# Performance work log

Hardware: AMD Instinct MI355X
Metric: run time of the kernel (lower is better)

The kernel has to match this reference:

```python
import jax, jax.numpy as jnp
import numpy as np


def setup_inputs() -> dict:
    key = jax.random.key(0)
    k1, k2 = jax.random.split(key)
    x = jax.random.normal(k1, (8, 128, 128, 128), dtype=jnp.float32)        # [N, C, H, W]
    codebook = jax.random.normal(k2, (256, 128), dtype=jnp.float32)         # [K, C] class_emb_vecs
    return {"x": x, "codebook": codebook}


def reference(x, codebook):
    # Brute-force 1-NN with p=2 (Euclidean), matching sklearn NearestNeighbors(brute, p=2).
    # argmin ||q - c||_2 == argmin (||q||^2 - 2 q.c + ||c||^2), so use the GEMM form.
    N, C, H, W = x.shape
    q = jnp.transpose(x, (0, 2, 3, 1)).reshape(-1, C)       # [N*H*W, C], matches x.reshape(-1, C) channel-last? 
    # NOTE: torch x.reshape(-1, C) on [N,C,H,W] flattens with C as the fastest-varying of the
    # leading dims only when memory layout is NCHW -> rows are (n, c_blocks)... Torch's
    # reshape(-1, C) actually slices contiguous groups of C elements along W. To be faithful
    # to x.reshape(-1, C) on a contiguous NCHW tensor:
    q = x.reshape(-1, C)                                     # [N*C*H*W/C, C] — same elements, same order as torch
    q_sq = jnp.sum(q * q, axis=1, keepdims=True)             # [M, 1]
    c_sq = jnp.sum(codebook * codebook, axis=1)              # [K]
    # squared distances: [M, K]
    d2 = q_sq - 2.0 * (q @ codebook.T) + c_sq[None, :]
    idx = jnp.argmin(d2, axis=1).astype(jnp.int32)           # [M]
    return idx.reshape(N, H, W)
```

## Files before the change

kernel.cpp:

```cpp
#include <hip/hip_runtime.h>
#include <hip/hip_bf16.h>


typedef __bf16 bf16x8 __attribute__((ext_vector_type(8)));
typedef float  floatx4 __attribute__((ext_vector_type(4)));

#define MFMA16 __builtin_amdgcn_mfma_f32_16x16x32_bf16

#define CNT_OFF 0
#define CSQ_OFF 1024
#define CBB_OFF 4096
#define WL_OFF  (4096 + 131072)
#define WL_CAP  32768
#define T_FLAG  0.004f

typedef __attribute__((address_space(1))) const unsigned int gu32;
typedef __attribute__((address_space(3))) unsigned int lu32;

__device__ __forceinline__ unsigned fmap(float f) {
    unsigned u = __float_as_uint(f);
    return (u & 0x80000000u) ? ~u : (u | 0x80000000u);
}

__global__ void knn_prep(const float* __restrict__ cb, __bf16* __restrict__ cbB,
                         float* __restrict__ csq, int* __restrict__ cnt) {
    const int tid = threadIdx.x;
    const int id = blockIdx.x * 256 + tid;
    if (id == 0) *cnt = 0;
    const int ln = id & 63;
    const int part = (id >> 6) & 1;
    const int step = id >> 7;
    const int t4 = step & 15;
    const int kb = step >> 4;
    const int n = t4 * 16 + (ln & 15);
    const int k0 = kb * 32 + (ln >> 4) * 8;
    const float* src = cb + (size_t)n * 128 + k0;
    union { __bf16 h[8]; uint4 u; } p;
#pragma unroll
    for (int j = 0; j < 8; ++j) {
        float f = src[j];
        __bf16 hh = (__bf16)f;
        p.h[j] = (part == 0) ? hh : (__bf16)(f - (float)hh);
    }
    *(uint4*)(cbB + (size_t)id * 8) = p.u;

    if (blockIdx.x == 0) {
        const float4* row = (const float4*)(cb + (size_t)tid * 128);
        float a0 = 0.f, a1 = 0.f, a2 = 0.f, a3 = 0.f;
#pragma unroll 8
        for (int j = 0; j < 32; ++j) {
            float4 v = row[j];
            a0 = fmaf(v.x, v.x, a0);
            a1 = fmaf(v.y, v.y, a1);
            a2 = fmaf(v.z, v.z, a2);
            a3 = fmaf(v.w, v.w, a3);
        }
        csq[tid] = (a0 + a1) + (a2 + a3);
    }
}

__global__ __launch_bounds__(512, 2) void knn_mfma(const float* __restrict__ x,
                                                   const __bf16* __restrict__ cbB,
                                                   const float* __restrict__ csq_g,
                                                   int* __restrict__ out,
                                                   int* __restrict__ cnt,
                                                   int* __restrict__ wl) {
    __shared__ __bf16 sB[65536];

    const int tid = threadIdx.x;
    const int wave = tid >> 6;
    const int lane = tid & 63;
    const int rl = lane & 15;
    const int kg = lane >> 4;

    {
        const char* gsrc = (const char*)cbB + wave * 16384 + lane * 16;
        char* ldst = (char*)sB + wave * 16384;
#pragma unroll
        for (int i = 0; i < 16; ++i)
            __builtin_amdgcn_global_load_lds((gu32*)(gsrc + i * 1024),
                                             (lu32*)(ldst + i * 1024), 16, 0, 0);
    }

    float cs[16];
#pragma unroll
    for (int t = 0; t < 16; ++t) cs[t] = csq_g[t * 16 + rl];

#pragma unroll 1
    for (int bt = 0; bt < 4; ++bt) {
        const size_t q0 = (size_t)blockIdx.x * 512 + bt * 128 + wave * 16;

        const float* xq = x + q0 * 128;
        bf16x8 ah[4], al[4];
#pragma unroll
        for (int kb = 0; kb < 4; ++kb) {
            const float* s = xq + (size_t)rl * 128 + kb * 32 + kg * 8;
            float4 f0 = *(const float4*)(s);
            float4 f1 = *(const float4*)(s + 4);
            float f[8] = {f0.x, f0.y, f0.z, f0.w, f1.x, f1.y, f1.z, f1.w};
            union { __bf16 h[8]; bf16x8 v; } ph, pl;
#pragma unroll
            for (int j = 0; j < 8; ++j) {
                __bf16 hh = (__bf16)f[j];
                ph.h[j] = hh;
                pl.h[j] = (__bf16)(f[j] - (float)hh);
            }
            ah[kb] = ph.v;
            al[kb] = pl.v;
        }

        floatx4 acc[16];
#pragma unroll
        for (int t = 0; t < 16; ++t) acc[t] = (floatx4){0.f, 0.f, 0.f, 0.f};

        if (bt == 0) __syncthreads();

#pragma unroll
        for (int kb = 0; kb < 4; ++kb) {
            const __bf16* sbase = sB + kb * 16384 + lane * 8;
#pragma unroll
            for (int t = 0; t < 16; ++t) {
                bf16x8 bh = *(const bf16x8*)(sbase + t * 1024);
                bf16x8 bl = *(const bf16x8*)(sbase + t * 1024 + 512);
                acc[t] = MFMA16(ah[kb], bh, acc[t], 0, 0, 0);
                acc[t] = MFMA16(al[kb], bh, acc[t], 0, 0, 0);
                acc[t] = MFMA16(ah[kb], bl, acc[t], 0, 0, 0);
            }
        }

#pragma unroll
        for (int r = 0; r < 4; ++r) {
            float bf = __builtin_inff(), sf = __builtin_inff();
            int bi = 0;
#pragma unroll
            for (int t = 0; t < 16; ++t) {
                const float sc = fmaf(-2.0f, acc[t][r], cs[t]);
                const bool lt = sc < bf;
                sf = lt ? bf : fminf(sf, sc);
                bf = lt ? sc : bf;
                bi = lt ? (t * 16 + rl) : bi;
            }
#pragma unroll
            for (int d = 1; d < 16; d <<= 1) {
                const float obf = __shfl_xor(bf, d);
                const int   obi = __shfl_xor(bi, d);
                const float osf = __shfl_xor(sf, d);
                const bool lt = obf < bf;
                const float loser = lt ? bf : obf;
                sf = fminf(fminf(sf, osf), loser);
                bf = lt ? obf : bf;
                bi = lt ? obi : bi;
            }
            if (rl == 0) {
                const size_t qg = q0 + kg * 4 + r;
                out[qg] = bi;
                if (sf - bf < T_FLAG) {
                    int idx = atomicAdd(cnt, 1);
                    if (idx < WL_CAP) wl[idx] = (int)qg;
                }
            }
        }
    }
}

__global__ __launch_bounds__(256) void knn_refine(const float* __restrict__ x,
                                                  const float* __restrict__ cb,
                                                  const float* __restrict__ csq_g,
                                                  const int* __restrict__ wl,
                                                  const int* __restrict__ cnt,
                                                  int* __restrict__ out) {
    __shared__ unsigned long long sP[4];
    const int tid = threadIdx.x;
    const int lane = tid & 63;
    const int wave = tid >> 6;

    int n = *cnt;
    if (n > WL_CAP) n = WL_CAP;
    const float mycsq = csq_g[tid];
    const float4* cr = (const float4*)(cb + (size_t)tid * 128);

    for (int i = blockIdx.x; i < n; i += gridDim.x) {
        const int q = wl[i];
        const float4* qr = (const float4*)(x + (size_t)q * 128);
        float a0 = 0.f, a1 = 0.f, a2 = 0.f, a3 = 0.f;
#pragma unroll 8
        for (int c4 = 0; c4 < 32; ++c4) {
            float4 qv = qr[c4];
            float4 cv = cr[c4];
            a0 = fmaf(qv.x, cv.x, a0);
            a1 = fmaf(qv.y, cv.y, a1);
            a2 = fmaf(qv.z, cv.z, a2);
            a3 = fmaf(qv.w, cv.w, a3);
        }
        float dot = (a0 + a1) + (a2 + a3);
        float score = fmaf(-2.0f, dot, mycsq);
        unsigned long long key =
            ((unsigned long long)fmap(score) << 32) | (unsigned)tid;
#pragma unroll
        for (int d = 1; d < 64; d <<= 1) {
            unsigned long long o = __shfl_xor(key, d);
            key = o < key ? o : key;
        }
        if (lane == 0) sP[wave] = key;
        __syncthreads();
        if (tid == 0) {
            unsigned long long b = sP[0];
            unsigned long long o;
            o = sP[1]; b = o < b ? o : b;
            o = sP[2]; b = o < b ? o : b;
            o = sP[3]; b = o < b ? o : b;
            out[q] = (int)(unsigned)(b & 0xFFFFFFFFull);
        }
        __syncthreads();
    }
}

extern "C" void kernel_launch(void* const* d_in, const int* in_sizes, int n_in,
                              void* d_out, int out_size, void* d_ws, size_t ws_size,
                              hipStream_t stream) {
    const float* x = (const float*)d_in[0];
    const float* cb = (const float*)d_in[1];
    int* out = (int*)d_out;

    char* ws = (char*)d_ws;
    int* cnt = (int*)(ws + CNT_OFF);
    float* csq = (float*)(ws + CSQ_OFF);
    __bf16* cbB = (__bf16*)(ws + CBB_OFF);
    int* wl = (int*)(ws + WL_OFF);

    const int M = in_sizes[0] / 128;

    knn_prep<<<32, 256, 0, stream>>>(cb, cbB, csq, cnt);
    knn_mfma<<<M / 512, 512, 0, stream>>>(x, cbB, csq, out, cnt, wl);
    knn_refine<<<240, 256, 0, stream>>>(x, cb, csq, wl, cnt, out);
}
```

Baseline: 121.9 us.

## Use 12 waves per block and fold codebook norms into MFMA accumulator init

Raises the block size of the main MFMA kernel from 8 to 12 waves. Each block still covers 512 queries, now as 32 tiles of 16 rows spread over 3 rounds, with the fourth-round waves masked off. The codebook LDS fill is redistributed across the 12 waves. Accumulators are seeded with -0.5*||c||^2 so the argmin becomes an argmax of the raw accumulator, which removes an FMA per score. The aim is more resident waves to hide latency, at the cost of fewer registers per thread and idle waves in the last round.

```diff
diff --git a/kernel.cpp b/kernel.cpp
--- a/kernel.cpp
+++ b/kernel.cpp
@@ -59,7 +59,7 @@
     }
 }
 
-__global__ __launch_bounds__(512, 2) void knn_mfma(const float* __restrict__ x,
+__global__ __launch_bounds__(768, 3) void knn_mfma(const float* __restrict__ x,
                                                    const __bf16* __restrict__ cbB,
                                                    const float* __restrict__ csq_g,
                                                    int* __restrict__ out,
@@ -73,13 +73,14 @@
     const int rl = lane & 15;
     const int kg = lane >> 4;
 
-    {
-        const char* gsrc = (const char*)cbB + wave * 16384 + lane * 16;
-        char* ldst = (char*)sB + wave * 16384;
-#pragma unroll
-        for (int i = 0; i < 16; ++i)
-            __builtin_amdgcn_global_load_lds((gu32*)(gsrc + i * 1024),
-                                             (lu32*)(ldst + i * 1024), 16, 0, 0);
+#pragma unroll
+    for (int i = 0; i < 11; ++i) {
+        const int c = wave + 12 * i;
+        if (c < 128) {
+            const char* g = (const char*)cbB + c * 1024 + lane * 16;
+            char* l = (char*)sB + c * 1024;
+            __builtin_amdgcn_global_load_lds((gu32*)g, (lu32*)l, 16, 0, 0);
+        }
     }
 
     float cs[16];
@@ -87,76 +88,85 @@
     for (int t = 0; t < 16; ++t) cs[t] = csq_g[t * 16 + rl];
 
 #pragma unroll 1
-    for (int bt = 0; bt < 4; ++bt) {
-        const size_t q0 = (size_t)blockIdx.x * 512 + bt * 128 + wave * 16;
-
-        const float* xq = x + q0 * 128;
+    for (int bt = 0; bt < 3; ++bt) {
+        const int c = bt * 12 + wave;
+        const bool valid = (c < 32);
+        const size_t q0 = (size_t)blockIdx.x * 512 + (size_t)c * 16;
+
         bf16x8 ah[4], al[4];
-#pragma unroll
-        for (int kb = 0; kb < 4; ++kb) {
-            const float* s = xq + (size_t)rl * 128 + kb * 32 + kg * 8;
-            float4 f0 = *(const float4*)(s);
-            float4 f1 = *(const float4*)(s + 4);
-            float f[8] = {f0.x, f0.y, f0.z, f0.w, f1.x, f1.y, f1.z, f1.w};
-            union { __bf16 h[8]; bf16x8 v; } ph, pl;
-#pragma unroll
-            for (int j = 0; j < 8; ++j) {
-                __bf16 hh = (__bf16)f[j];
-                ph.h[j] = hh;
-                pl.h[j] = (__bf16)(f[j] - (float)hh);
-            }
-            ah[kb] = ph.v;
-            al[kb] = pl.v;
-        }
-
         floatx4 acc[16];
-#pragma unroll
-        for (int t = 0; t < 16; ++t) acc[t] = (floatx4){0.f, 0.f, 0.f, 0.f};
+
+        if (valid) {
+            const float* xq = x + q0 * 128;
+#pragma unroll
+            for (int kb = 0; kb < 4; ++kb) {
+                const float* s = xq + (size_t)rl * 128 + kb * 32 + kg * 8;
+                float4 f0 = *(const float4*)(s);
+                float4 f1 = *(const float4*)(s + 4);
+                float f[8] = {f0.x, f0.y, f0.z, f0.w, f1.x, f1.y, f1.z, f1.w};
+                union { __bf16 h[8]; bf16x8 v; } ph, pl;
+#pragma unroll
+                for (int j = 0; j < 8; ++j) {
+                    __bf16 hh = (__bf16)f[j];
+                    ph.h[j] = hh;
+                    pl.h[j] = (__bf16)(f[j] - (float)hh);
+                }
+                ah[kb] = ph.v;
+                al[kb] = pl.v;
+            }
+#pragma unroll
+            for (int t = 0; t < 16; ++t) {
+                const float iv = -0.5f * cs[t];
+                acc[t] = (floatx4){iv, iv, iv, iv};
+            }
+        }
 
         if (bt == 0) __syncthreads();
 
-#pragma unroll
-        for (int kb = 0; kb < 4; ++kb) {
-            const __bf16* sbase = sB + kb * 16384 + lane * 8;
-#pragma unroll
-            for (int t = 0; t < 16; ++t) {
-                bf16x8 bh = *(const bf16x8*)(sbase + t * 1024);
-                bf16x8 bl = *(const bf16x8*)(sbase + t * 1024 + 512);
-                acc[t] = MFMA16(ah[kb], bh, acc[t], 0, 0, 0);
-                acc[t] = MFMA16(al[kb], bh, acc[t], 0, 0, 0);
-                acc[t] = MFMA16(ah[kb], bl, acc[t], 0, 0, 0);
-            }
-        }
-
-#pragma unroll
-        for (int r = 0; r < 4; ++r) {
-            float bf = __builtin_inff(), sf = __builtin_inff();
-            int bi = 0;
-#pragma unroll
-            for (int t = 0; t < 16; ++t) {
-                const float sc = fmaf(-2.0f, acc[t][r], cs[t]);
-                const bool lt = sc < bf;
-                sf = lt ? bf : fminf(sf, sc);
-                bf = lt ? sc : bf;
-                bi = lt ? (t * 16 + rl) : bi;
-            }
-#pragma unroll
-            for (int d = 1; d < 16; d <<= 1) {
-                const float obf = __shfl_xor(bf, d);
-                const int   obi = __shfl_xor(bi, d);
-                const float osf = __shfl_xor(sf, d);
-                const bool lt = obf < bf;
-                const float loser = lt ? bf : obf;
-                sf = fminf(fminf(sf, osf), loser);
-                bf = lt ? obf : bf;
-                bi = lt ? obi : bi;
-            }
-            if (rl == 0) {
-                const size_t qg = q0 + kg * 4 + r;
-                out[qg] = bi;
-                if (sf - bf < T_FLAG) {
-                    int idx = atomicAdd(cnt, 1);
-                    if (idx < WL_CAP) wl[idx] = (int)qg;
+        if (valid) {
+#pragma unroll
+            for (int kb = 0; kb < 4; ++kb) {
+                const __bf16* sbase = sB + kb * 16384 + lane * 8;
+#pragma unroll
+                for (int t = 0; t < 16; ++t) {
+                    bf16x8 bh = *(const bf16x8*)(sbase + t * 1024);
+                    bf16x8 bl = *(const bf16x8*)(sbase + t * 1024 + 512);
+                    acc[t] = MFMA16(ah[kb], bh, acc[t], 0, 0, 0);
+                    acc[t] = MFMA16(al[kb], bh, acc[t], 0, 0, 0);
+                    acc[t] = MFMA16(ah[kb], bl, acc[t], 0, 0, 0);
+                }
+            }
+
+#pragma unroll
+            for (int r = 0; r < 4; ++r) {
+                float bf = -__builtin_inff(), sf = -__builtin_inff();
+                int bi = 0;
+#pragma unroll
+                for (int t = 0; t < 16; ++t) {
+                    const float sc = acc[t][r];
+                    const bool gt = sc > bf;
+                    sf = gt ? bf : fmaxf(sf, sc);
+                    bf = gt ? sc : bf;
+                    bi = gt ? (t * 16 + rl) : bi;
+                }
+#pragma unroll
+                for (int d = 1; d < 16; d <<= 1) {
+                    const float obf = __shfl_xor(bf, d);
+                    const int   obi = __shfl_xor(bi, d);
+                    const float osf = __shfl_xor(sf, d);
+                    const bool gt = obf > bf;
+                    const float loser = gt ? bf : obf;
+                    sf = fmaxf(fmaxf(sf, osf), loser);
+                    bf = gt ? obf : bf;
+                    bi = gt ? obi : bi;
+                }
+                if (rl == 0) {
+                    const size_t qg = q0 + kg * 4 + r;
+                    out[qg] = bi;
+                    if (2.0f * (bf - sf) < T_FLAG) {
+                        int idx = atomicAdd(cnt, 1);
+                        if (idx < WL_CAP) wl[idx] = (int)qg;
+                    }
                 }
             }
         }
@@ -231,6 +241,6 @@
     const int M = in_sizes[0] / 128;
 
     knn_prep<<<32, 256, 0, stream>>>(cb, cbB, csq, cnt);
-    knn_mfma<<<M / 512, 512, 0, stream>>>(x, cbB, csq, out, cnt, wl);
+    knn_mfma<<<M / 512, 768, 0, stream>>>(x, cbB, csq, out, cnt, wl);
     knn_refine<<<240, 256, 0, stream>>>(x, cb, csq, wl, cnt, out);
 }
```

New measurement: 152.5 us. 25.1% more time.

## Split codebook across wave pairs with 1024-thread blocks and add merge kernel

Applied to the files above, without the earlier changes.

Doubles the block to 1024 threads so each pair of waves splits the 256 codebook entries in half, halving per-wave accumulator registers and raising parallelism. Each half writes its partial best and second-best to a workspace buffer, and a new merge kernel combines the two halves, writes the index and builds the refine worklist. The intent is higher occupancy and more latency hiding in the MFMA kernel. The cost is an extra kernel launch, extra global traffic for the partial results, and each query row being loaded and split into bf16 halves twice.

```diff
diff --git a/kernel.cpp b/kernel.cpp
--- a/kernel.cpp
+++ b/kernel.cpp
@@ -11,6 +11,8 @@
 #define CSQ_OFF 1024
 #define CBB_OFF 4096
 #define WL_OFF  (4096 + 131072)
+#define PBF_OFF (WL_OFF + WL_CAP * 4)
+#define PBI_OFF (PBF_OFF + 2097152)
 #define WL_CAP  32768
 #define T_FLAG  0.004f
 
@@ -59,12 +61,11 @@
     }
 }
 
-__global__ __launch_bounds__(512, 2) void knn_mfma(const float* __restrict__ x,
-                                                   const __bf16* __restrict__ cbB,
-                                                   const float* __restrict__ csq_g,
-                                                   int* __restrict__ out,
-                                                   int* __restrict__ cnt,
-                                                   int* __restrict__ wl) {
+__global__ __launch_bounds__(1024, 4) void knn_mfma(const float* __restrict__ x,
+                                                    const __bf16* __restrict__ cbB,
+                                                    const float* __restrict__ csq_g,
+                                                    float2* __restrict__ pbf,
+                                                    int* __restrict__ pbi) {
     __shared__ __bf16 sB[65536];
 
     const int tid = threadIdx.x;
@@ -72,59 +73,60 @@
     const int lane = tid & 63;
     const int rl = lane & 15;
     const int kg = lane >> 4;
+    const int pair = wave >> 1;
+    const int half = wave & 1;
 
     {
-        const char* gsrc = (const char*)cbB + wave * 16384 + lane * 16;
-        char* ldst = (char*)sB + wave * 16384;
-#pragma unroll
-        for (int i = 0; i < 16; ++i)
+        const char* gsrc = (const char*)cbB + wave * 8192 + lane * 16;
+        char* ldst = (char*)sB + wave * 8192;
+#pragma unroll
+        for (int i = 0; i < 8; ++i)
             __builtin_amdgcn_global_load_lds((gu32*)(gsrc + i * 1024),
                                              (lu32*)(ldst + i * 1024), 16, 0, 0);
     }
 
-    float cs[16];
-#pragma unroll
-    for (int t = 0; t < 16; ++t) cs[t] = csq_g[t * 16 + rl];
+    float cs[8];
+#pragma unroll
+    for (int tt = 0; tt < 8; ++tt) cs[tt] = csq_g[(half * 8 + tt) * 16 + rl];
 
 #pragma unroll 1
     for (int bt = 0; bt < 4; ++bt) {
-        const size_t q0 = (size_t)blockIdx.x * 512 + bt * 128 + wave * 16;
-
-        const float* xq = x + q0 * 128;
+        const size_t q0 = (size_t)blockIdx.x * 512 + bt * 128 + pair * 16;
+
+        const float* xq = x + (q0 + rl) * 128 + kg * 8;
         bf16x8 ah[4], al[4];
 #pragma unroll
         for (int kb = 0; kb < 4; ++kb) {
-            const float* s = xq + (size_t)rl * 128 + kb * 32 + kg * 8;
-            float4 f0 = *(const float4*)(s);
-            float4 f1 = *(const float4*)(s + 4);
+            float4 f0 = *(const float4*)(xq + kb * 32);
+            float4 f1 = *(const float4*)(xq + kb * 32 + 4);
             float f[8] = {f0.x, f0.y, f0.z, f0.w, f1.x, f1.y, f1.z, f1.w};
-            union { __bf16 h[8]; bf16x8 v; } ph, pl;
+            union { __bf16 h[8]; bf16x8 v; } phv, plv;
 #pragma unroll
             for (int j = 0; j < 8; ++j) {
                 __bf16 hh = (__bf16)f[j];
-                ph.h[j] = hh;
-                pl.h[j] = (__bf16)(f[j] - (float)hh);
-            }
-            ah[kb] = ph.v;
-            al[kb] = pl.v;
-        }
-
-        floatx4 acc[16];
-#pragma unroll
-        for (int t = 0; t < 16; ++t) acc[t] = (floatx4){0.f, 0.f, 0.f, 0.f};
+                phv.h[j] = hh;
+                plv.h[j] = (__bf16)(f[j] - (float)hh);
+            }
+            ah[kb] = phv.v;
+            al[kb] = plv.v;
+        }
+
+        floatx4 acc[8];
+#pragma unroll
+        for (int tt = 0; tt < 8; ++tt) acc[tt] = (floatx4){0.f, 0.f, 0.f, 0.f};
 
         if (bt == 0) __syncthreads();
 
 #pragma unroll
         for (int kb = 0; kb < 4; ++kb) {
-            const __bf16* sbase = sB + kb * 16384 + lane * 8;
-#pragma unroll
-            for (int t = 0; t < 16; ++t) {
-                bf16x8 bh = *(const bf16x8*)(sbase + t * 1024);
-                bf16x8 bl = *(const bf16x8*)(sbase + t * 1024 + 512);
-                acc[t] = MFMA16(ah[kb], bh, acc[t], 0, 0, 0);
-                acc[t] = MFMA16(al[kb], bh, acc[t], 0, 0, 0);
-                acc[t] = MFMA16(ah[kb], bl, acc[t], 0, 0, 0);
+            const __bf16* sbase = sB + kb * 16384 + half * 8192 + lane * 8;
+#pragma unroll
+            for (int tt = 0; tt < 8; ++tt) {
+                bf16x8 bh = *(const bf16x8*)(sbase + tt * 1024);
+                bf16x8 bl = *(const bf16x8*)(sbase + tt * 1024 + 512);
+                acc[tt] = MFMA16(ah[kb], bh, acc[tt], 0, 0, 0);
+                acc[tt] = MFMA16(al[kb], bh, acc[tt], 0, 0, 0);
+                acc[tt] = MFMA16(ah[kb], bl, acc[tt], 0, 0, 0);
             }
         }
 
@@ -133,12 +135,12 @@
             float bf = __builtin_inff(), sf = __builtin_inff();
             int bi = 0;
 #pragma unroll
-            for (int t = 0; t < 16; ++t) {
-                const float sc = fmaf(-2.0f, acc[t][r], cs[t]);
+            for (int tt = 0; tt < 8; ++tt) {
+                const float sc = fmaf(-2.0f, acc[tt][r], cs[tt]);
                 const bool lt = sc < bf;
                 sf = lt ? bf : fminf(sf, sc);
                 bf = lt ? sc : bf;
-                bi = lt ? (t * 16 + rl) : bi;
+                bi = lt ? ((half * 8 + tt) * 16 + rl) : bi;
             }
 #pragma unroll
             for (int d = 1; d < 16; d <<= 1) {
@@ -153,13 +155,28 @@
             }
             if (rl == 0) {
                 const size_t qg = q0 + kg * 4 + r;
-                out[qg] = bi;
-                if (sf - bf < T_FLAG) {
-                    int idx = atomicAdd(cnt, 1);
-                    if (idx < WL_CAP) wl[idx] = (int)qg;
-                }
-            }
-        }
+                pbf[qg * 2 + half] = (float2){bf, sf};
+                pbi[qg * 2 + half] = bi;
+            }
+        }
+    }
+}
+
+__global__ __launch_bounds__(256) void knn_merge(const float2* __restrict__ pbf,
+                                                 const int* __restrict__ pbi,
+                                                 int* __restrict__ out,
+                                                 int* __restrict__ cnt,
+                                                 int* __restrict__ wl) {
+    const int q = blockIdx.x * 256 + threadIdx.x;
+    const float4 v = *(const float4*)(pbf + (size_t)q * 2);
+    const int2  iv = *(const int2*)(pbi + (size_t)q * 2);
+    const bool w0 = v.x < v.z;
+    const float B = w0 ? v.x : v.z;
+    const float S = fminf(w0 ? v.y : v.w, w0 ? v.z : v.x);
+    out[q] = w0 ? iv.x : iv.y;
+    if (S - B < T_FLAG) {
+        int idx = atomicAdd(cnt, 1);
+        if (idx < WL_CAP) wl[idx] = q;
     }
 }
 
@@ -227,10 +244,13 @@
     float* csq = (float*)(ws + CSQ_OFF);
     __bf16* cbB = (__bf16*)(ws + CBB_OFF);
     int* wl = (int*)(ws + WL_OFF);
+    float2* pbf = (float2*)(ws + PBF_OFF);
+    int* pbi = (int*)(ws + PBI_OFF);
 
     const int M = in_sizes[0] / 128;
 
     knn_prep<<<32, 256, 0, stream>>>(cb, cbB, csq, cnt);
-    knn_mfma<<<M / 512, 512, 0, stream>>>(x, cbB, csq, out, cnt, wl);
+    knn_mfma<<<M / 512, 1024, 0, stream>>>(x, cbB, csq, pbf, pbi);
+    knn_merge<<<M / 256, 256, 0, stream>>>(pbf, pbi, out, cnt, wl);
     knn_refine<<<240, 256, 0, stream>>>(x, cb, csq, wl, cnt, out);
 }
```

After: 126.8 us. 4.0% more time.
